# Kernel optimization log

Measured on AMD Instinct MI355X. Metric: run time of the kernel, lower is better.

Reference implementation:

```python
import jax, jax.numpy as jnp
import numpy as np

WBITS_MAX = 3.0   # 3-bit signed narrow-range weights: levels in [-3, 3]
ABITS_MAX = 15.0  # 4-bit unsigned activations: levels in [0, 15]


def round_ste(x):
    # straight-through estimator for round (Brevitas uses STE)
    return x + jax.lax.stop_gradient(jnp.round(x) - x)


def quant_weight(w):
    # per-tensor symmetric narrow-range 3-bit fake quant (Int weight per-tensor float)
    s = jnp.max(jnp.abs(w)) / WBITS_MAX
    wq = jnp.clip(round_ste(w / s), -WBITS_MAX, WBITS_MAX) * s
    return wq, s


def quant_bias(b, w_scale, in_step):
    # Brevitas BiasQuant: bias scale = input_scale * weight_scale, no clipping (wide int)
    sb = w_scale * in_step  # in_step is shape (1,)
    return round_ste(b / sb) * sb


def quant_relu(x, s):
    # QuantReLU(bit_width=4): relu then unsigned 4-bit fake quant with learned scale s
    step = s / ABITS_MAX
    return jnp.clip(round_ste(jax.nn.relu(x) / step), 0.0, ABITS_MAX) * step


def conv2d(x, w):
    return jax.lax.conv_general_dilated(
        x, w, window_strides=(1, 1), padding='VALID',
        dimension_numbers=('NCHW', 'OIHW', 'NCHW'))


def maxpool2(x):
    return jax.lax.reduce_window(x, -jnp.inf, jax.lax.max,
                                 (1, 1, 2, 2), (1, 1, 2, 2), 'VALID')


def setup_inputs() -> dict:
    key = jax.random.key(0)
    ks = jax.random.split(key, 16)
    d = {}
    d['x'] = jax.random.normal(ks[0], (256, 3, 160, 160), jnp.float32)
    d['w1'] = jax.random.normal(ks[1], (6, 3, 3, 3), jnp.float32) * 0.2
    d['w2'] = jax.random.normal(ks[2], (12, 6, 3, 3), jnp.float32) * 0.2
    d['b2'] = jax.random.normal(ks[3], (12,), jnp.float32) * 0.1
    d['w3'] = jax.random.normal(ks[4], (18, 12, 3, 3), jnp.float32) * 0.2
    d['b3'] = jax.random.normal(ks[5], (18,), jnp.float32) * 0.1
    d['w4'] = jax.random.normal(ks[6], (18, 18, 3, 3), jnp.float32) * 0.2
    d['b4'] = jax.random.normal(ks[7], (18,), jnp.float32) * 0.1
    d['w5'] = jax.random.normal(ks[8], (18, 18, 3, 3), jnp.float32) * 0.2
    d['b5'] = jax.random.normal(ks[9], (18,), jnp.float32) * 0.1
    d['fw1'] = jax.random.normal(ks[10], (120, 162), jnp.float32) * 0.1
    d['fb1'] = jax.random.normal(ks[11], (120,), jnp.float32) * 0.1
    d['fw2'] = jax.random.normal(ks[12], (84, 120), jnp.float32) * 0.1
    d['fb2'] = jax.random.normal(ks[13], (84,), jnp.float32) * 0.1
    d['fw3'] = jax.random.normal(ks[14], (9, 84), jnp.float32) * 0.1
    for i in range(1, 8):
        d[f's{i}'] = jnp.full((1,), 6.0, jnp.float32)  # learned act scales (calibrated init)
    return d


def reference(x, w1, w2, b2, w3, b3, w4, b4, w5, b5,
              fw1, fb1, fw2, fb2, fw3, s1, s2, s3, s4, s5, s6, s7):
    # stage 1 (note: original forward feeds raw x into conv1, bypassing quant_inp)
    q1, _ = quant_weight(w1)
    out = maxpool2(quant_relu(conv2d(x, q1), s1))            # [B,6,79,79]
    # stage 2
    q2, ws2 = quant_weight(w2)
    bq2 = quant_bias(b2, ws2, s1 / ABITS_MAX)
    out = maxpool2(quant_relu(conv2d(out, q2) + bq2[None, :, None, None], s2))  # [B,12,38,38]
    # stage 3
    q3, ws3 = quant_weight(w3)
    bq3 = quant_bias(b3, ws3, s2 / ABITS_MAX)
    out = maxpool2(quant_relu(conv2d(out, q3) + bq3[None, :, None, None], s3))  # [B,18,18,18]
    # stage 4
    q4, ws4 = quant_weight(w4)
    bq4 = quant_bias(b4, ws4, s3 / ABITS_MAX)
    out = maxpool2(quant_relu(conv2d(out, q4) + bq4[None, :, None, None], s4))  # [B,18,8,8]
    # stage 5
    q5, ws5 = quant_weight(w5)
    bq5 = quant_bias(b5, ws5, s4 / ABITS_MAX)
    out = maxpool2(quant_relu(conv2d(out, q5) + bq5[None, :, None, None], s5))  # [B,18,3,3]
    out = out.reshape(out.shape[0], -1)                      # [B,162]
    # fc1
    qf1, fs1 = quant_weight(fw1)
    bqf1 = quant_bias(fb1, fs1, s5 / ABITS_MAX)
    out = quant_relu(out @ qf1.T + bqf1, s6)                 # [B,120]
    # fc2
    qf2, fs2 = quant_weight(fw2)
    bqf2 = quant_bias(fb2, fs2, s6 / ABITS_MAX)
    out = quant_relu(out @ qf2.T + bqf2, s7)                 # [B,84]
    # fc3 (no bias, output not re-quantized: return_quant_tensor=False default path)
    qf3, _ = quant_weight(fw3)
    return out @ qf3.T                                       # [B,9]
```

## Files before the change

kernel.cpp:

```cpp
#include <hip/hip_runtime.h>
#include <hip/hip_bf16.h>
#include <math.h>
#include <type_traits>

constexpr size_t OFF_OUT1B = 0;
constexpr size_t OFF_OUT2B = (size_t)256 * 6 * 79 * 80;

template<int CIN, int COUT, int NCO, int HIN, int WSIN,
         int HPOOL, int WPOOL, int WSOUT, int XG, int RB,
         int THREADS, bool HAS_BIAS, bool IN_U8>
__global__ __launch_bounds__(THREADS)
void conv_stage(const void* __restrict__ in_,
                const float* __restrict__ w_raw,
                const float* __restrict__ b_raw,
                const float* __restrict__ s_prev,
                const float* __restrict__ s_act,
                unsigned char* __restrict__ out)
{
    using TIN = typename std::conditional<IN_U8, unsigned char, float>::type;
    constexpr int GROUPS = COUT / NCO;
    constexpr int W4IN   = WSIN / 4;
    constexpr int NW     = COUT * CIN * 9;
    constexpr int STEPS  = 4 * CIN;
    static_assert(NCO * GROUPS == COUT, "NCO divides COUT");
    static_assert(GROUPS * XG * RB <= THREADS, "single compute pass");
    static_assert(4 * XG == WSOUT, "full padded row coverage");
    static_assert(WSIN % 4 == 0, "vec4 loads");

    __shared__ float lw[NW];
    __shared__ float lb[COUT];
    __shared__ float red[THREADS];

    const int r0  = blockIdx.x * RB;
    const int n   = blockIdx.y;
    const int tid = threadIdx.x;

    float mx = 0.0f;
    for (int i = tid; i < NW; i += THREADS) {
        const float v = w_raw[i];
        lw[i] = v;
        mx = fmaxf(mx, fabsf(v));
    }
    if (HAS_BIAS)
        for (int i = tid; i < COUT; i += THREADS) lb[i] = b_raw[i];
    red[tid] = mx;
    __syncthreads();
    for (int s = THREADS / 2; s > 0; s >>= 1) {
        if (tid < s) red[tid] = fmaxf(red[tid], red[tid + s]);
        __syncthreads();
    }
    const float sw_ = red[0] / 3.0f;
    for (int i = tid; i < NW; i += THREADS) {
        float q = rintf(lw[i] / sw_);
        q = fminf(fmaxf(q, -3.0f), 3.0f);
        lw[i] = q * sw_;
    }
    if (HAS_BIAS) {
        const float sb = sw_ * (s_prev[0] / 15.0f);
        for (int i = tid; i < COUT; i += THREADS)
            lb[i] = rintf(lb[i] / sb) * sb;
    }
    __syncthreads();

    const int o = tid;
    if (o >= GROUPS * XG * RB) return;
    const int cog = o % GROUPS;
    const int xg  = (o / GROUPS) % XG;
    const int ry  = o / (GROUPS * XG);
    const int r   = r0 + ry;
    if (r >= HPOOL) return;

    const float step = s_act[0] / 15.0f;
    float step_in = 0.0f;
    if constexpr (IN_U8) step_in = s_prev[0] / 15.0f;

    const int u0 = 2 * xg;
    const int u1 = 2 * xg + 1;
    const int u2 = (2 * xg + 2 < W4IN) ? (2 * xg + 2) : (W4IN - 1);

    const TIN* in   = (const TIN*)in_;
    const TIN* base = in + (size_t)n * CIN * HIN * WSIN + (size_t)(2 * r) * WSIN;

    float acc[NCO][16];
#pragma unroll
    for (int j = 0; j < NCO; ++j)
#pragma unroll
        for (int i = 0; i < 16; ++i) acc[j][i] = 0.0f;

    float4       fbuf[3][3];
    unsigned int ubuf[3][3];
    float        wv[NCO][9];

#define ISSUE_STEP(S)                                                          \
    {                                                                          \
        const TIN* rp = base + (size_t)((S) >> 2) * HIN * WSIN                 \
                             + (size_t)((S) & 3) * WSIN;                       \
        if constexpr (IN_U8) {                                                 \
            ubuf[(S) % 3][0] = *(const unsigned int*)&rp[4 * u0];              \
            ubuf[(S) % 3][1] = *(const unsigned int*)&rp[4 * u1];              \
            ubuf[(S) % 3][2] = *(const unsigned int*)&rp[4 * u2];              \
        } else {                                                               \
            fbuf[(S) % 3][0] = *(const float4*)&rp[4 * u0];                    \
            fbuf[(S) % 3][1] = *(const float4*)&rp[4 * u1];                    \
            fbuf[(S) % 3][2] = *(const float4*)&rp[4 * u2];                    \
        }                                                                      \
    }

    ISSUE_STEP(0);
    ISSUE_STEP(1);

#pragma unroll
    for (int s = 0; s < STEPS; ++s) {
        const int c  = s >> 2;
        const int rr = s & 3;

        if (s + 2 < STEPS) ISSUE_STEP(s + 2);

        if (rr == 0) {
#pragma unroll
            for (int j = 0; j < NCO; ++j)
#pragma unroll
                for (int k = 0; k < 9; ++k)
                    wv[j][k] = lw[((NCO * cog + j) * CIN + c) * 9 + k];
        }

        float row[12];
        if constexpr (IN_U8) {
#pragma unroll
            for (int k = 0; k < 3; ++k) {
                const unsigned int d = ubuf[s % 3][k];
#pragma unroll
                for (int b = 0; b < 4; ++b)
                    row[4 * k + b] = (float)((d >> (8 * b)) & 0xffu) * step_in;
            }
        } else {
            const float* rv = (const float*)fbuf[s % 3];
#pragma unroll
            for (int i = 0; i < 12; ++i) row[i] = rv[i];
        }

        if (rr < 3) {
#pragma unroll
            for (int j = 0; j < NCO; ++j)
#pragma unroll
                for (int kc = 0; kc < 3; ++kc)
#pragma unroll
                    for (int xx = 0; xx < 8; ++xx)
                        acc[j][xx] = fmaf(row[xx + kc], wv[j][rr * 3 + kc], acc[j][xx]);
        }
        if (rr >= 1) {
#pragma unroll
            for (int j = 0; j < NCO; ++j)
#pragma unroll
                for (int kc = 0; kc < 3; ++kc)
#pragma unroll
                    for (int xx = 0; xx < 8; ++xx)
                        acc[j][8 + xx] = fmaf(row[xx + kc], wv[j][(rr - 1) * 3 + kc], acc[j][8 + xx]);
        }
    }
#undef ISSUE_STEP

#pragma unroll
    for (int j = 0; j < NCO; ++j) {
        const int co = NCO * cog + j;
        const float bias = HAS_BIAS ? lb[co] : 0.0f;
        unsigned int pck = 0;
#pragma unroll
        for (int t = 0; t < 4; ++t) {
            float m = fmaxf(fmaxf(acc[j][2 * t], acc[j][2 * t + 1]),
                            fmaxf(acc[j][8 + 2 * t], acc[j][8 + 2 * t + 1]));
            float v = fmaxf(m + bias, 0.0f);
            float q = rintf(v / step);
            q = fminf(fmaxf(q, 0.0f), 15.0f);
            const unsigned int qi = (4 * xg + t < WPOOL) ? (unsigned int)q : 0u;
            pck |= qi << (8 * t);
        }
        *(unsigned int*)&out[(((size_t)n * COUT + co) * HPOOL + r) * WSOUT + 4 * xg] = pck;
    }
}

__device__ __forceinline__ float wave_max(float v) {
#pragma unroll
    for (int off = 32; off > 0; off >>= 1)
        v = fmaxf(v, __shfl_down(v, off));
    return v;
}

__global__ __launch_bounds__(1024)
void tail_mega(const unsigned char* __restrict__ in2,
               const float* __restrict__ w3, const float* __restrict__ b3,
               const float* __restrict__ w4, const float* __restrict__ b4,
               const float* __restrict__ w5, const float* __restrict__ b5,
               const float* __restrict__ fw1, const float* __restrict__ fb1,
               const float* __restrict__ fw2, const float* __restrict__ fb2,
               const float* __restrict__ fw3,
               const float* __restrict__ s2, const float* __restrict__ s3,
               const float* __restrict__ s4, const float* __restrict__ s5,
               const float* __restrict__ s6, const float* __restrict__ s7,
               float* __restrict__ out)
{
    __shared__ unsigned int SLu[4560];
    __shared__ float A3[5832];
    __shared__ float W3q[1944], W4q[2916], W5q[2916];
    __shared__ float B3q[18], B4q[18], B5q[18];
    __shared__ float O4[1152];
    __shared__ float A5[162], A6[120], A7[84];
    __shared__ float sm[16][6];
    __shared__ float scales[6];

    const int n    = blockIdx.x;
    const int tid  = threadIdx.x;
    const int wid  = tid >> 6;
    const int lane = tid & 63;

    {
        const uint4* src = (const uint4*)(in2 + (size_t)n * 18240);
        uint4* dst = (uint4*)SLu;
        for (int i = tid; i < 1140; i += 1024) dst[i] = src[i];
    }
    float m3 = 0.f, m4 = 0.f, m5 = 0.f, g1 = 0.f, g2 = 0.f, g3 = 0.f;
    for (int i = tid; i < 1944; i += 1024) { const float v = w3[i]; W3q[i] = v; m3 = fmaxf(m3, fabsf(v)); }
    for (int i = tid; i < 2916; i += 1024) { const float v = w4[i]; W4q[i] = v; m4 = fmaxf(m4, fabsf(v)); }
    for (int i = tid; i < 2916; i += 1024) { const float v = w5[i]; W5q[i] = v; m5 = fmaxf(m5, fabsf(v)); }
    {
        const float4* f1 = (const float4*)fw1;
        for (int i = tid; i < 4860; i += 1024) {
            const float4 v = f1[i];
            g1 = fmaxf(g1, fmaxf(fmaxf(fabsf(v.x), fabsf(v.y)), fmaxf(fabsf(v.z), fabsf(v.w))));
        }
        const float4* f2 = (const float4*)fw2;
        for (int i = tid; i < 2520; i += 1024) {
            const float4 v = f2[i];
            g2 = fmaxf(g2, fmaxf(fmaxf(fabsf(v.x), fabsf(v.y)), fmaxf(fabsf(v.z), fabsf(v.w))));
        }
        const float4* f3 = (const float4*)fw3;
        for (int i = tid; i < 189; i += 1024) {
            const float4 v = f3[i];
            g3 = fmaxf(g3, fmaxf(fmaxf(fabsf(v.x), fabsf(v.y)), fmaxf(fabsf(v.z), fabsf(v.w))));
        }
    }
    if (tid < 18) { B3q[tid] = b3[tid]; B4q[tid] = b4[tid]; B5q[tid] = b5[tid]; }
    m3 = wave_max(m3); m4 = wave_max(m4); m5 = wave_max(m5);
    g1 = wave_max(g1); g2 = wave_max(g2); g3 = wave_max(g3);
    if (lane == 0) {
        sm[wid][0] = m3; sm[wid][1] = m4; sm[wid][2] = m5;
        sm[wid][3] = g1; sm[wid][4] = g2; sm[wid][5] = g3;
    }
    __syncthreads();
    if (tid < 6) {
        float v = sm[0][tid];
#pragma unroll
        for (int w = 1; w < 16; ++w) v = fmaxf(v, sm[w][tid]);
        scales[tid] = v / 3.0f;
    }
    __syncthreads();
    const float sw3 = scales[0], sw4 = scales[1], sw5 = scales[2];
    const float sf1 = scales[3], sf2 = scales[4], sf3 = scales[5];

    for (int i = tid; i < 1944; i += 1024) { float q = rintf(W3q[i] / sw3); q = fminf(fmaxf(q, -3.f), 3.f); W3q[i] = q * sw3; }
    for (int i = tid; i < 2916; i += 1024) { float q = rintf(W4q[i] / sw4); q = fminf(fmaxf(q, -3.f), 3.f); W4q[i] = q * sw4; }
    for (int i = tid; i < 2916; i += 1024) { float q = rintf(W5q[i] / sw5); q = fminf(fmaxf(q, -3.f), 3.f); W5q[i] = q * sw5; }
    if (tid < 18) {
        const float sb3 = sw3 * (s2[0] / 15.0f); B3q[tid] = rintf(B3q[tid] / sb3) * sb3;
        const float sb4 = sw4 * (s3[0] / 15.0f); B4q[tid] = rintf(B4q[tid] / sb4) * sb4;
        const float sb5 = sw5 * (s4[0] / 15.0f); B5q[tid] = rintf(B5q[tid] / sb5) * sb5;
    }
    __syncthreads();

    {
        const unsigned char* SLb = (const unsigned char*)SLu;
        const float step2 = s2[0] / 15.0f;
        const float st = s3[0] / 15.0f;
        if (tid < 972) {
            const int r  = tid / 54;
            const int rm = tid - r * 54;
            const int co = rm / 3;
            const int th = rm - co * 3;

            float acc0[12], acc1[12];
#pragma unroll
            for (int i = 0; i < 12; ++i) { acc0[i] = 0.f; acc1[i] = 0.f; }

            for (int c = 0; c < 12; ++c) {
                float wvv[9];
#pragma unroll
                for (int k = 0; k < 9; ++k) wvv[k] = W3q[(co * 12 + c) * 9 + k];
#pragma unroll
                for (int rr = 0; rr < 4; ++rr) {
                    const int off = (c * 38 + 2 * r + rr) * 40 + 12 * th;
                    float row[16];
#pragma unroll
                    for (int k = 0; k < 4; ++k) {
                        const unsigned int d = *(const unsigned int*)&SLb[off + 4 * k];
#pragma unroll
                        for (int b = 0; b < 4; ++b)
                            row[4 * k + b] = (float)((d >> (8 * b)) & 0xffu) * step2;
                    }
                    if (rr < 3) {
#pragma unroll
                        for (int kc = 0; kc < 3; ++kc)
#pragma unroll
                            for (int xx = 0; xx < 12; ++xx)
                                acc0[xx] = fmaf(row[xx + kc], wvv[rr * 3 + kc], acc0[xx]);
                    }
                    if (rr >= 1) {
#pragma unroll
                        for (int kc = 0; kc < 3; ++kc)
#pragma unroll
                            for (int xx = 0; xx < 12; ++xx)
                                acc1[xx] = fmaf(row[xx + kc], wvv[(rr - 1) * 3 + kc], acc1[xx]);
                    }
                }
            }
            const float bias = B3q[co];
#pragma unroll
            for (int x = 0; x < 6; ++x) {
                float m = fmaxf(fmaxf(acc0[2 * x], acc0[2 * x + 1]),
                                fmaxf(acc1[2 * x], acc1[2 * x + 1]));
                float v = fmaxf(m + bias, 0.0f);
                float q = rintf(v / st);
                q = fminf(fmaxf(q, 0.0f), 15.0f);
                A3[(co * 18 + r) * 18 + 6 * th + x] = q * st;
            }
        }
    }
    __syncthreads();

    {
        const float st = s4[0] / 15.0f;
        for (int o = tid; o < 1152; o += 1024) {
            const int co = o >> 6;
            const int r  = (o >> 3) & 7;
            const int x  = o & 7;
            float a00 = 0.f, a01 = 0.f, a10 = 0.f, a11 = 0.f;
            for (int c = 0; c < 18; ++c) {
                float win[4][4];
#pragma unroll
                for (int rr = 0; rr < 4; ++rr) {
                    const int base = c * 324 + (2 * r + rr) * 18 + 2 * x;
                    *(float2*)&win[rr][0] = *(const float2*)&A3[base];
                    *(float2*)&win[rr][2] = *(const float2*)&A3[base + 2];
                }
                const float* wp = &W4q[(co * 18 + c) * 9];
#pragma unroll
                for (int kr = 0; kr < 3; ++kr)
#pragma unroll
                    for (int kc = 0; kc < 3; ++kc) {
                        const float wvv = wp[kr * 3 + kc];
                        a00 = fmaf(win[kr    ][kc    ], wvv, a00);
                        a01 = fmaf(win[kr    ][kc + 1], wvv, a01);
                        a10 = fmaf(win[kr + 1][kc    ], wvv, a10);
                        a11 = fmaf(win[kr + 1][kc + 1], wvv, a11);
                    }
            }
            float m = fmaxf(fmaxf(a00, a01), fmaxf(a10, a11));
            float v = fmaxf(m + B4q[co], 0.0f);
            float q = rintf(v / st);
            q = fminf(fmaxf(q, 0.0f), 15.0f);
            O4[o] = q * st;
        }
    }
    __syncthreads();

    {
        const float st = s5[0] / 15.0f;
        if (tid < 162) {
            const int co  = tid / 9;
            const int rem = tid - co * 9;
            const int r   = rem / 3;
            const int x   = rem - r * 3;
            float a00 = 0.f, a01 = 0.f, a10 = 0.f, a11 = 0.f;
            for (int c = 0; c < 18; ++c) {
                float win[4][4];
#pragma unroll
                for (int rr = 0; rr < 4; ++rr) {
                    const int base = c * 64 + (2 * r + rr) * 8 + 2 * x;
                    *(float2*)&win[rr][0] = *(const float2*)&O4[base];
                    *(float2*)&win[rr][2] = *(const float2*)&O4[base + 2];
                }
                const float* wp = &W5q[(co * 18 + c) * 9];
#pragma unroll
                for (int kr = 0; kr < 3; ++kr)
#pragma unroll
                    for (int kc = 0; kc < 3; ++kc) {
                        const float wvv = wp[kr * 3 + kc];
                        a00 = fmaf(win[kr    ][kc    ], wvv, a00);
                        a01 = fmaf(win[kr    ][kc + 1], wvv, a01);
                        a10 = fmaf(win[kr + 1][kc    ], wvv, a10);
                        a11 = fmaf(win[kr + 1][kc + 1], wvv, a11);
                    }
            }
            float m = fmaxf(fmaxf(a00, a01), fmaxf(a10, a11));
            float v = fmaxf(m + B5q[co], 0.0f);
            float q = rintf(v / st);
            q = fminf(fmaxf(q, 0.0f), 15.0f);
            A5[tid] = q * st;
        }
    }
    __syncthreads();

    if (tid < 120) {
        float acc = 0.f;
        const float* wr = fw1 + (size_t)tid * 162;
#pragma unroll 6
        for (int k = 0; k < 162; ++k) {
            float q = rintf(wr[k] / sf1);
            q = fminf(fmaxf(q, -3.f), 3.f);
            acc = fmaf(A5[k], q * sf1, acc);
        }
        const float sb = sf1 * (s5[0] / 15.0f);
        acc += rintf(fb1[tid] / sb) * sb;
        const float st = s6[0] / 15.0f;
        float q = rintf(fmaxf(acc, 0.0f) / st);
        q = fminf(fmaxf(q, 0.0f), 15.0f);
        A6[tid] = q * st;
    }
    __syncthreads();

    if (tid < 84) {
        float acc = 0.f;
        const float* wr = fw2 + (size_t)tid * 120;
#pragma unroll 6
        for (int k = 0; k < 120; ++k) {
            float q = rintf(wr[k] / sf2);
            q = fminf(fmaxf(q, -3.f), 3.f);
            acc = fmaf(A6[k], q * sf2, acc);
        }
        const float sb = sf2 * (s6[0] / 15.0f);
        acc += rintf(fb2[tid] / sb) * sb;
        const float st = s7[0] / 15.0f;
        float q = rintf(fmaxf(acc, 0.0f) / st);
        q = fminf(fmaxf(q, 0.0f), 15.0f);
        A7[tid] = q * st;
    }
    __syncthreads();

    if (tid < 9) {
        float acc = 0.f;
        const float* wr = fw3 + (size_t)tid * 84;
#pragma unroll 6
        for (int k = 0; k < 84; ++k) {
            float q = rintf(wr[k] / sf3);
            q = fminf(fmaxf(q, -3.f), 3.f);
            acc = fmaf(A7[k], q * sf3, acc);
        }
        out[(size_t)n * 9 + tid] = acc;
    }
}

extern "C" void kernel_launch(void* const* d_in, const int* in_sizes, int n_in,
                              void* d_out, int out_size, void* d_ws, size_t ws_size,
                              hipStream_t stream)
{
    const float* x   = (const float*)d_in[0];
    const float* w1  = (const float*)d_in[1];
    const float* w2  = (const float*)d_in[2];
    const float* b2  = (const float*)d_in[3];
    const float* w3  = (const float*)d_in[4];
    const float* b3  = (const float*)d_in[5];
    const float* w4  = (const float*)d_in[6];
    const float* b4  = (const float*)d_in[7];
    const float* w5  = (const float*)d_in[8];
    const float* b5  = (const float*)d_in[9];
    const float* fw1 = (const float*)d_in[10];
    const float* fb1 = (const float*)d_in[11];
    const float* fw2 = (const float*)d_in[12];
    const float* fb2 = (const float*)d_in[13];
    const float* fw3 = (const float*)d_in[14];
    const float* s1  = (const float*)d_in[15];
    const float* s2  = (const float*)d_in[16];
    const float* s3  = (const float*)d_in[17];
    const float* s4  = (const float*)d_in[18];
    const float* s5  = (const float*)d_in[19];
    const float* s6  = (const float*)d_in[20];
    const float* s7  = (const float*)d_in[21];

    unsigned char* wsb = (unsigned char*)d_ws;
    float* out = (float*)d_out;

    conv_stage<3, 6, 2, 160, 160, 79, 79, 80, 20, 4, 256, false, false>
        <<<dim3(20, 256), 256, 0, stream>>>(x, w1, nullptr, nullptr, s1,
                                            wsb + OFF_OUT1B);

    conv_stage<6, 12, 2, 79, 80, 38, 38, 40, 10, 4, 256, true, true>
        <<<dim3(10, 256), 256, 0, stream>>>(wsb + OFF_OUT1B, w2, b2, s1, s2,
                                            wsb + OFF_OUT2B);

    tail_mega<<<256, 1024, 0, stream>>>(wsb + OFF_OUT2B,
                                        w3, b3, w4, b4, w5, b5,
                                        fw1, fb1, fw2, fb2, fw3,
                                        s2, s3, s4, s5, s6, s7, out);
}
```

Measured before the change: 138.9 us.

## Split stage-3 conv into its own kernel and parallelize FC layers across K-chunks

Moves the stage-3 convolution out of the per-image tail kernel into a separate kernel with two row blocks per image, so 512 blocks instead of 256 share the work. Inputs are decoded to float once in LDS and read as float4, and the results go to workspace as float. The remaining tail kernel reads A3 from global memory, stores O4 channel-last with padding, and splits the three FC dot products across up to 8 K-chunks with a shared-memory partial reduction. The cost is an extra launch and a float A3 round trip through global memory, and w3's absmax is recomputed in every block.

```diff
diff --git a/kernel.cpp b/kernel.cpp
--- a/kernel.cpp
+++ b/kernel.cpp
@@ -5,6 +5,7 @@
 
 constexpr size_t OFF_OUT1B = 0;
 constexpr size_t OFF_OUT2B = (size_t)256 * 6 * 79 * 80;
+constexpr size_t OFF_A3B   = 0;
 
 template<int CIN, int COUT, int NCO, int HIN, int WSIN,
          int HPOOL, int WPOOL, int WSOUT, int XG, int RB,
@@ -186,27 +187,138 @@
     return v;
 }
 
+__global__ __launch_bounds__(512)
+void conv3_stage(const unsigned char* __restrict__ in2,
+                 const float* __restrict__ w3, const float* __restrict__ b3,
+                 const float* __restrict__ s2, const float* __restrict__ s3,
+                 float* __restrict__ a3)
+{
+    __shared__ float SLf[12 * 20 * 40];
+    __shared__ float lw[1944];
+    __shared__ float lb[18];
+    __shared__ float red[512];
+
+    const int rb  = blockIdx.x;
+    const int n   = blockIdx.y;
+    const int tid = threadIdx.x;
+
+    float mx = 0.0f;
+    for (int i = tid; i < 1944; i += 512) {
+        const float v = w3[i];
+        lw[i] = v;
+        mx = fmaxf(mx, fabsf(v));
+    }
+    if (tid < 18) lb[tid] = b3[tid];
+    red[tid] = mx;
+
+    const float step2 = s2[0] / 15.0f;
+    {
+        const unsigned char* src = in2 + (size_t)n * 18240;
+        for (int d = tid; d < 2400; d += 512) {
+            const int c    = d / 200;
+            const int rem  = d - c * 200;
+            const int lrow = rem / 10;
+            const int dw   = rem - lrow * 10;
+            const unsigned int u =
+                *(const unsigned int*)&src[c * 1520 + (18 * rb + lrow) * 40 + 4 * dw];
+            float* q = &SLf[(c * 20 + lrow) * 40 + 4 * dw];
+            q[0] = (float)(u & 0xffu) * step2;
+            q[1] = (float)((u >> 8) & 0xffu) * step2;
+            q[2] = (float)((u >> 16) & 0xffu) * step2;
+            q[3] = (float)(u >> 24) * step2;
+        }
+    }
+    __syncthreads();
+    for (int s = 256; s > 0; s >>= 1) {
+        if (tid < s) red[tid] = fmaxf(red[tid], red[tid + s]);
+        __syncthreads();
+    }
+    const float sw = red[0] / 3.0f;
+    for (int i = tid; i < 1944; i += 512) {
+        float q = rintf(lw[i] / sw);
+        q = fminf(fmaxf(q, -3.0f), 3.0f);
+        lw[i] = q * sw;
+    }
+    if (tid < 18) {
+        const float sb = sw * (s2[0] / 15.0f);
+        lb[tid] = rintf(lb[tid] / sb) * sb;
+    }
+    __syncthreads();
+
+    if (tid >= 486) return;
+    const int rloc = tid / 54;
+    const int rm   = tid - rloc * 54;
+    const int co   = rm / 3;
+    const int th   = rm - co * 3;
+    const int r    = rb * 9 + rloc;
+
+    const float st = s3[0] / 15.0f;
+
+    float acc0[12], acc1[12];
+#pragma unroll
+    for (int i = 0; i < 12; ++i) { acc0[i] = 0.f; acc1[i] = 0.f; }
+
+    for (int c = 0; c < 12; ++c) {
+        float wv[9];
+#pragma unroll
+        for (int k = 0; k < 9; ++k) wv[k] = lw[(co * 12 + c) * 9 + k];
+#pragma unroll
+        for (int rr = 0; rr < 4; ++rr) {
+            const float* rp = &SLf[(c * 20 + 2 * rloc + rr) * 40 + 12 * th];
+            float4 rv[4];
+#pragma unroll
+            for (int v = 0; v < 4; ++v) rv[v] = *(const float4*)&rp[4 * v];
+            const float* row = (const float*)rv;
+            if (rr < 3) {
+#pragma unroll
+                for (int kc = 0; kc < 3; ++kc)
+#pragma unroll
+                    for (int xx = 0; xx < 12; ++xx)
+                        acc0[xx] = fmaf(row[xx + kc], wv[rr * 3 + kc], acc0[xx]);
+            }
+            if (rr >= 1) {
+#pragma unroll
+                for (int kc = 0; kc < 3; ++kc)
+#pragma unroll
+                    for (int xx = 0; xx < 12; ++xx)
+                        acc1[xx] = fmaf(row[xx + kc], wv[(rr - 1) * 3 + kc], acc1[xx]);
+            }
+        }
+    }
+
+    const float bias = lb[co];
+    float* orow = a3 + (size_t)n * 5832 + (size_t)co * 324 + (size_t)r * 18 + 6 * th;
+#pragma unroll
+    for (int x = 0; x < 6; ++x) {
+        float m = fmaxf(fmaxf(acc0[2 * x], acc0[2 * x + 1]),
+                        fmaxf(acc1[2 * x], acc1[2 * x + 1]));
+        float v = fmaxf(m + bias, 0.0f);
+        float q = rintf(v / st);
+        q = fminf(fmaxf(q, 0.0f), 15.0f);
+        orow[x] = q * st;
+    }
+}
+
 __global__ __launch_bounds__(1024)
-void tail_mega(const unsigned char* __restrict__ in2,
-               const float* __restrict__ w3, const float* __restrict__ b3,
-               const float* __restrict__ w4, const float* __restrict__ b4,
-               const float* __restrict__ w5, const float* __restrict__ b5,
-               const float* __restrict__ fw1, const float* __restrict__ fb1,
-               const float* __restrict__ fw2, const float* __restrict__ fb2,
-               const float* __restrict__ fw3,
-               const float* __restrict__ s2, const float* __restrict__ s3,
-               const float* __restrict__ s4, const float* __restrict__ s5,
-               const float* __restrict__ s6, const float* __restrict__ s7,
-               float* __restrict__ out)
+void tail456(const float* __restrict__ a3in,
+             const float* __restrict__ w4, const float* __restrict__ b4,
+             const float* __restrict__ w5, const float* __restrict__ b5,
+             const float* __restrict__ fw1, const float* __restrict__ fb1,
+             const float* __restrict__ fw2, const float* __restrict__ fb2,
+             const float* __restrict__ fw3,
+             const float* __restrict__ s3, const float* __restrict__ s4,
+             const float* __restrict__ s5, const float* __restrict__ s6,
+             const float* __restrict__ s7,
+             float* __restrict__ out)
 {
-    __shared__ unsigned int SLu[4560];
     __shared__ float A3[5832];
-    __shared__ float W3q[1944], W4q[2916], W5q[2916];
-    __shared__ float B3q[18], B4q[18], B5q[18];
-    __shared__ float O4[1152];
+    __shared__ float W4q[2916], W5q[2916];
+    __shared__ float B4q[18], B5q[18];
+    __shared__ float O4t[64 * 19 + 1];
     __shared__ float A5[162], A6[120], A7[84];
-    __shared__ float sm[16][6];
-    __shared__ float scales[6];
+    __shared__ float part[8][120];
+    __shared__ float sm[16][5];
+    __shared__ float scales[5];
 
     const int n    = blockIdx.x;
     const int tid  = threadIdx.x;
@@ -214,12 +326,11 @@
     const int lane = tid & 63;
 
     {
-        const uint4* src = (const uint4*)(in2 + (size_t)n * 18240);
-        uint4* dst = (uint4*)SLu;
-        for (int i = tid; i < 1140; i += 1024) dst[i] = src[i];
-    }
-    float m3 = 0.f, m4 = 0.f, m5 = 0.f, g1 = 0.f, g2 = 0.f, g3 = 0.f;
-    for (int i = tid; i < 1944; i += 1024) { const float v = w3[i]; W3q[i] = v; m3 = fmaxf(m3, fabsf(v)); }
+        const float4* src = (const float4*)(a3in + (size_t)n * 5832);
+        float4* dst = (float4*)A3;
+        for (int i = tid; i < 1458; i += 1024) dst[i] = src[i];
+    }
+    float m4 = 0.f, m5 = 0.f, g1 = 0.f, g2 = 0.f, g3 = 0.f;
     for (int i = tid; i < 2916; i += 1024) { const float v = w4[i]; W4q[i] = v; m4 = fmaxf(m4, fabsf(v)); }
     for (int i = tid; i < 2916; i += 1024) { const float v = w5[i]; W5q[i] = v; m5 = fmaxf(m5, fabsf(v)); }
     {
@@ -239,90 +350,29 @@
             g3 = fmaxf(g3, fmaxf(fmaxf(fabsf(v.x), fabsf(v.y)), fmaxf(fabsf(v.z), fabsf(v.w))));
         }
     }
-    if (tid < 18) { B3q[tid] = b3[tid]; B4q[tid] = b4[tid]; B5q[tid] = b5[tid]; }
-    m3 = wave_max(m3); m4 = wave_max(m4); m5 = wave_max(m5);
+    if (tid < 18) { B4q[tid] = b4[tid]; B5q[tid] = b5[tid]; }
+    m4 = wave_max(m4); m5 = wave_max(m5);
     g1 = wave_max(g1); g2 = wave_max(g2); g3 = wave_max(g3);
     if (lane == 0) {
-        sm[wid][0] = m3; sm[wid][1] = m4; sm[wid][2] = m5;
-        sm[wid][3] = g1; sm[wid][4] = g2; sm[wid][5] = g3;
-    }
-    __syncthreads();
-    if (tid < 6) {
+        sm[wid][0] = m4; sm[wid][1] = m5;
+        sm[wid][2] = g1; sm[wid][3] = g2; sm[wid][4] = g3;
+    }
+    __syncthreads();
+    if (tid < 5) {
         float v = sm[0][tid];
 #pragma unroll
         for (int w = 1; w < 16; ++w) v = fmaxf(v, sm[w][tid]);
         scales[tid] = v / 3.0f;
     }
     __syncthreads();
-    const float sw3 = scales[0], sw4 = scales[1], sw5 = scales[2];
-    const float sf1 = scales[3], sf2 = scales[4], sf3 = scales[5];
-
-    for (int i = tid; i < 1944; i += 1024) { float q = rintf(W3q[i] / sw3); q = fminf(fmaxf(q, -3.f), 3.f); W3q[i] = q * sw3; }
+    const float sw4 = scales[0], sw5 = scales[1];
+    const float sf1 = scales[2], sf2 = scales[3], sf3 = scales[4];
+
     for (int i = tid; i < 2916; i += 1024) { float q = rintf(W4q[i] / sw4); q = fminf(fmaxf(q, -3.f), 3.f); W4q[i] = q * sw4; }
     for (int i = tid; i < 2916; i += 1024) { float q = rintf(W5q[i] / sw5); q = fminf(fmaxf(q, -3.f), 3.f); W5q[i] = q * sw5; }
     if (tid < 18) {
-        const float sb3 = sw3 * (s2[0] / 15.0f); B3q[tid] = rintf(B3q[tid] / sb3) * sb3;
         const float sb4 = sw4 * (s3[0] / 15.0f); B4q[tid] = rintf(B4q[tid] / sb4) * sb4;
         const float sb5 = sw5 * (s4[0] / 15.0f); B5q[tid] = rintf(B5q[tid] / sb5) * sb5;
-    }
-    __syncthreads();
-
-    {
-        const unsigned char* SLb = (const unsigned char*)SLu;
-        const float step2 = s2[0] / 15.0f;
-        const float st = s3[0] / 15.0f;
-        if (tid < 972) {
-            const int r  = tid / 54;
-            const int rm = tid - r * 54;
-            const int co = rm / 3;
-            const int th = rm - co * 3;
-
-            float acc0[12], acc1[12];
-#pragma unroll
-            for (int i = 0; i < 12; ++i) { acc0[i] = 0.f; acc1[i] = 0.f; }
-
-            for (int c = 0; c < 12; ++c) {
-                float wvv[9];
-#pragma unroll
-                for (int k = 0; k < 9; ++k) wvv[k] = W3q[(co * 12 + c) * 9 + k];
-#pragma unroll
-                for (int rr = 0; rr < 4; ++rr) {
-                    const int off = (c * 38 + 2 * r + rr) * 40 + 12 * th;
-                    float row[16];
-#pragma unroll
-                    for (int k = 0; k < 4; ++k) {
-                        const unsigned int d = *(const unsigned int*)&SLb[off + 4 * k];
-#pragma unroll
-                        for (int b = 0; b < 4; ++b)
-                            row[4 * k + b] = (float)((d >> (8 * b)) & 0xffu) * step2;
-                    }
-                    if (rr < 3) {
-#pragma unroll
-                        for (int kc = 0; kc < 3; ++kc)
-#pragma unroll
-                            for (int xx = 0; xx < 12; ++xx)
-                                acc0[xx] = fmaf(row[xx + kc], wvv[rr * 3 + kc], acc0[xx]);
-                    }
-                    if (rr >= 1) {
-#pragma unroll
-                        for (int kc = 0; kc < 3; ++kc)
-#pragma unroll
-                            for (int xx = 0; xx < 12; ++xx)
-                                acc1[xx] = fmaf(row[xx + kc], wvv[(rr - 1) * 3 + kc], acc1[xx]);
-                    }
-                }
-            }
-            const float bias = B3q[co];
-#pragma unroll
-            for (int x = 0; x < 6; ++x) {
-                float m = fmaxf(fmaxf(acc0[2 * x], acc0[2 * x + 1]),
-                                fmaxf(acc1[2 * x], acc1[2 * x + 1]));
-                float v = fmaxf(m + bias, 0.0f);
-                float q = rintf(v / st);
-                q = fminf(fmaxf(q, 0.0f), 15.0f);
-                A3[(co * 18 + r) * 18 + 6 * th + x] = q * st;
-            }
-        }
     }
     __syncthreads();
 
@@ -357,7 +407,7 @@
             float v = fmaxf(m + B4q[co], 0.0f);
             float q = rintf(v / st);
             q = fminf(fmaxf(q, 0.0f), 15.0f);
-            O4[o] = q * st;
+            O4t[(r * 8 + x) * 19 + co] = q * st;
         }
     }
     __syncthreads();
@@ -373,11 +423,10 @@
             for (int c = 0; c < 18; ++c) {
                 float win[4][4];
 #pragma unroll
-                for (int rr = 0; rr < 4; ++rr) {
-                    const int base = c * 64 + (2 * r + rr) * 8 + 2 * x;
-                    *(float2*)&win[rr][0] = *(const float2*)&O4[base];
-                    *(float2*)&win[rr][2] = *(const float2*)&O4[base + 2];
-                }
+                for (int rr = 0; rr < 4; ++rr)
+#pragma unroll
+                    for (int cc = 0; cc < 4; ++cc)
+                        win[rr][cc] = O4t[((2 * r + rr) * 8 + 2 * x + cc) * 19 + c];
                 const float* wp = &W5q[(co * 18 + c) * 9];
 #pragma unroll
                 for (int kr = 0; kr < 3; ++kr)
@@ -399,15 +448,25 @@
     }
     __syncthreads();
 
-    if (tid < 120) {
-        float acc = 0.f;
-        const float* wr = fw1 + (size_t)tid * 162;
-#pragma unroll 6
-        for (int k = 0; k < 162; ++k) {
+    if (tid < 960) {
+        const int m  = tid % 120;
+        const int ch = tid / 120;
+        const int k0 = 21 * ch;
+        const int k1 = (ch == 7) ? 162 : k0 + 21;
+        float p = 0.f;
+        const float* wr = fw1 + (size_t)m * 162;
+        for (int k = k0; k < k1; ++k) {
             float q = rintf(wr[k] / sf1);
             q = fminf(fmaxf(q, -3.f), 3.f);
-            acc = fmaf(A5[k], q * sf1, acc);
-        }
+            p = fmaf(A5[k], q * sf1, p);
+        }
+        part[ch][m] = p;
+    }
+    __syncthreads();
+    if (tid < 120) {
+        float acc = part[0][tid];
+#pragma unroll
+        for (int ch = 1; ch < 8; ++ch) acc += part[ch][tid];
         const float sb = sf1 * (s5[0] / 15.0f);
         acc += rintf(fb1[tid] / sb) * sb;
         const float st = s6[0] / 15.0f;
@@ -417,15 +476,24 @@
     }
     __syncthreads();
 
-    if (tid < 84) {
-        float acc = 0.f;
-        const float* wr = fw2 + (size_t)tid * 120;
-#pragma unroll 6
-        for (int k = 0; k < 120; ++k) {
+    if (tid < 672) {
+        const int m  = tid % 84;
+        const int ch = tid / 84;
+        const int k0 = 15 * ch;
+        float p = 0.f;
+        const float* wr = fw2 + (size_t)m * 120;
+        for (int k = k0; k < k0 + 15; ++k) {
             float q = rintf(wr[k] / sf2);
             q = fminf(fmaxf(q, -3.f), 3.f);
-            acc = fmaf(A6[k], q * sf2, acc);
-        }
+            p = fmaf(A6[k], q * sf2, p);
+        }
+        part[ch][m] = p;
+    }
+    __syncthreads();
+    if (tid < 84) {
+        float acc = part[0][tid];
+#pragma unroll
+        for (int ch = 1; ch < 8; ++ch) acc += part[ch][tid];
         const float sb = sf2 * (s6[0] / 15.0f);
         acc += rintf(fb2[tid] / sb) * sb;
         const float st = s7[0] / 15.0f;
@@ -435,15 +503,24 @@
     }
     __syncthreads();
 
-    if (tid < 9) {
-        float acc = 0.f;
-        const float* wr = fw3 + (size_t)tid * 84;
-#pragma unroll 6
-        for (int k = 0; k < 84; ++k) {
+    if (tid < 63) {
+        const int m  = tid % 9;
+        const int ch = tid / 9;
+        const int k0 = 12 * ch;
+        float p = 0.f;
+        const float* wr = fw3 + (size_t)m * 84;
+        for (int k = k0; k < k0 + 12; ++k) {
             float q = rintf(wr[k] / sf3);
             q = fminf(fmaxf(q, -3.f), 3.f);
-            acc = fmaf(A7[k], q * sf3, acc);
-        }
+            p = fmaf(A7[k], q * sf3, p);
+        }
+        part[ch][m] = p;
+    }
+    __syncthreads();
+    if (tid < 9) {
+        float acc = part[0][tid];
+#pragma unroll
+        for (int ch = 1; ch < 7; ++ch) acc += part[ch][tid];
         out[(size_t)n * 9 + tid] = acc;
     }
 }
@@ -486,8 +563,11 @@
         <<<dim3(10, 256), 256, 0, stream>>>(wsb + OFF_OUT1B, w2, b2, s1, s2,
                                             wsb + OFF_OUT2B);
 
-    tail_mega<<<256, 1024, 0, stream>>>(wsb + OFF_OUT2B,
-                                        w3, b3, w4, b4, w5, b5,
-                                        fw1, fb1, fw2, fb2, fw3,
-                                        s2, s3, s4, s5, s6, s7, out);
+    conv3_stage<<<dim3(2, 256), 512, 0, stream>>>(wsb + OFF_OUT2B, w3, b3, s2, s3,
+                                                  (float*)(wsb + OFF_A3B));
+
+    tail456<<<256, 1024, 0, stream>>>((const float*)(wsb + OFF_A3B),
+                                      w4, b4, w5, b5,
+                                      fw1, fb1, fw2, fb2, fw3,
+                                      s3, s4, s5, s6, s7, out);
 }
```

Measured after the change: 141.8 us. +2.1%, slower.

## Stream stage-3 input from global with double buffering; split FC reductions across threads

Applied to the files above, without the earlier changes.

The tail kernel no longer stages the stage-2 activations in shared memory. Each thread loads its input rows straight from global memory into registers, double-buffered per input channel, so the loads overlap with the FMAs. The A3 and O4 shared arrays get padded or transposed layouts, and the three FC layers split their K dimension across up to 8 thread chunks with a shared-memory reduction. This cuts shared-memory footprint and the serial FC tail, at the cost of more registers and some uncoalesced global loads.

```diff
diff --git a/kernel.cpp b/kernel.cpp
--- a/kernel.cpp
+++ b/kernel.cpp
@@ -187,24 +187,24 @@
 }
 
 __global__ __launch_bounds__(1024)
-void tail_mega(const unsigned char* __restrict__ in2,
-               const float* __restrict__ w3, const float* __restrict__ b3,
-               const float* __restrict__ w4, const float* __restrict__ b4,
-               const float* __restrict__ w5, const float* __restrict__ b5,
-               const float* __restrict__ fw1, const float* __restrict__ fb1,
-               const float* __restrict__ fw2, const float* __restrict__ fb2,
-               const float* __restrict__ fw3,
-               const float* __restrict__ s2, const float* __restrict__ s3,
-               const float* __restrict__ s4, const float* __restrict__ s5,
-               const float* __restrict__ s6, const float* __restrict__ s7,
-               float* __restrict__ out)
+void tail_all(const unsigned char* __restrict__ in2,
+              const float* __restrict__ w3, const float* __restrict__ b3,
+              const float* __restrict__ w4, const float* __restrict__ b4,
+              const float* __restrict__ w5, const float* __restrict__ b5,
+              const float* __restrict__ fw1, const float* __restrict__ fb1,
+              const float* __restrict__ fw2, const float* __restrict__ fb2,
+              const float* __restrict__ fw3,
+              const float* __restrict__ s2, const float* __restrict__ s3,
+              const float* __restrict__ s4, const float* __restrict__ s5,
+              const float* __restrict__ s6, const float* __restrict__ s7,
+              float* __restrict__ out)
 {
-    __shared__ unsigned int SLu[4560];
-    __shared__ float A3[5832];
+    __shared__ float A3f[18 * 18 * 20];
     __shared__ float W3q[1944], W4q[2916], W5q[2916];
     __shared__ float B3q[18], B4q[18], B5q[18];
-    __shared__ float O4[1152];
+    __shared__ float O4t[64 * 19 + 1];
     __shared__ float A5[162], A6[120], A7[84];
+    __shared__ float part[8][120];
     __shared__ float sm[16][6];
     __shared__ float scales[6];
 
@@ -213,11 +213,6 @@
     const int wid  = tid >> 6;
     const int lane = tid & 63;
 
-    {
-        const uint4* src = (const uint4*)(in2 + (size_t)n * 18240);
-        uint4* dst = (uint4*)SLu;
-        for (int i = tid; i < 1140; i += 1024) dst[i] = src[i];
-    }
     float m3 = 0.f, m4 = 0.f, m5 = 0.f, g1 = 0.f, g2 = 0.f, g3 = 0.f;
     for (int i = tid; i < 1944; i += 1024) { const float v = w3[i]; W3q[i] = v; m3 = fmaxf(m3, fabsf(v)); }
     for (int i = tid; i < 2916; i += 1024) { const float v = w4[i]; W4q[i] = v; m4 = fmaxf(m4, fabsf(v)); }
@@ -267,61 +262,78 @@
     }
     __syncthreads();
 
-    {
-        const unsigned char* SLb = (const unsigned char*)SLu;
+    if (tid < 972) {
+        const int r  = tid / 54;
+        const int rm = tid - r * 54;
+        const int co = rm / 3;
+        const int th = rm - co * 3;
+
         const float step2 = s2[0] / 15.0f;
-        const float st = s3[0] / 15.0f;
-        if (tid < 972) {
-            const int r  = tid / 54;
-            const int rm = tid - r * 54;
-            const int co = rm / 3;
-            const int th = rm - co * 3;
-
-            float acc0[12], acc1[12];
-#pragma unroll
-            for (int i = 0; i < 12; ++i) { acc0[i] = 0.f; acc1[i] = 0.f; }
-
-            for (int c = 0; c < 12; ++c) {
-                float wvv[9];
-#pragma unroll
-                for (int k = 0; k < 9; ++k) wvv[k] = W3q[(co * 12 + c) * 9 + k];
-#pragma unroll
-                for (int rr = 0; rr < 4; ++rr) {
-                    const int off = (c * 38 + 2 * r + rr) * 40 + 12 * th;
-                    float row[16];
-#pragma unroll
-                    for (int k = 0; k < 4; ++k) {
-                        const unsigned int d = *(const unsigned int*)&SLb[off + 4 * k];
-#pragma unroll
-                        for (int b = 0; b < 4; ++b)
-                            row[4 * k + b] = (float)((d >> (8 * b)) & 0xffu) * step2;
-                    }
-                    if (rr < 3) {
-#pragma unroll
-                        for (int kc = 0; kc < 3; ++kc)
-#pragma unroll
-                            for (int xx = 0; xx < 12; ++xx)
-                                acc0[xx] = fmaf(row[xx + kc], wvv[rr * 3 + kc], acc0[xx]);
-                    }
-                    if (rr >= 1) {
-#pragma unroll
-                        for (int kc = 0; kc < 3; ++kc)
-#pragma unroll
-                            for (int xx = 0; xx < 12; ++xx)
-                                acc1[xx] = fmaf(row[xx + kc], wvv[(rr - 1) * 3 + kc], acc1[xx]);
-                    }
+        const float st3   = s3[0] / 15.0f;
+        const unsigned char* base = in2 + (size_t)n * 18240 + (size_t)(2 * r) * 40 + 12 * th;
+
+        float acc0[12], acc1[12];
+#pragma unroll
+        for (int i = 0; i < 12; ++i) { acc0[i] = 0.f; acc1[i] = 0.f; }
+
+        uint4 ub[2][4];
+
+#define LOADC(C, B)                                                            \
+        {                                                                      \
+            const unsigned char* cp = base + (size_t)(C) * 1520;               \
+            _Pragma("unroll")                                                  \
+            for (int rr = 0; rr < 4; ++rr)                                     \
+                __builtin_memcpy(&ub[B][rr], cp + rr * 40, 16);                \
+        }
+
+        LOADC(0, 0);
+
+#pragma unroll
+        for (int c = 0; c < 12; ++c) {
+            if (c + 1 < 12) LOADC(c + 1, (c + 1) & 1);
+
+            float wv[9];
+#pragma unroll
+            for (int k = 0; k < 9; ++k) wv[k] = W3q[(co * 12 + c) * 9 + k];
+
+#pragma unroll
+            for (int rr = 0; rr < 4; ++rr) {
+                const unsigned int* dp = (const unsigned int*)&ub[c & 1][rr];
+                float row[16];
+#pragma unroll
+                for (int k = 0; k < 4; ++k) {
+                    const unsigned int d = dp[k];
+#pragma unroll
+                    for (int b = 0; b < 4; ++b)
+                        row[4 * k + b] = (float)((d >> (8 * b)) & 0xffu) * step2;
+                }
+                if (rr < 3) {
+#pragma unroll
+                    for (int kc = 0; kc < 3; ++kc)
+#pragma unroll
+                        for (int xx = 0; xx < 12; ++xx)
+                            acc0[xx] = fmaf(row[xx + kc], wv[rr * 3 + kc], acc0[xx]);
+                }
+                if (rr >= 1) {
+#pragma unroll
+                    for (int kc = 0; kc < 3; ++kc)
+#pragma unroll
+                        for (int xx = 0; xx < 12; ++xx)
+                            acc1[xx] = fmaf(row[xx + kc], wv[(rr - 1) * 3 + kc], acc1[xx]);
                 }
             }
-            const float bias = B3q[co];
-#pragma unroll
-            for (int x = 0; x < 6; ++x) {
-                float m = fmaxf(fmaxf(acc0[2 * x], acc0[2 * x + 1]),
-                                fmaxf(acc1[2 * x], acc1[2 * x + 1]));
-                float v = fmaxf(m + bias, 0.0f);
-                float q = rintf(v / st);
-                q = fminf(fmaxf(q, 0.0f), 15.0f);
-                A3[(co * 18 + r) * 18 + 6 * th + x] = q * st;
-            }
+        }
+#undef LOADC
+
+        const float bias = B3q[co];
+#pragma unroll
+        for (int x = 0; x < 6; ++x) {
+            float m = fmaxf(fmaxf(acc0[2 * x], acc0[2 * x + 1]),
+                            fmaxf(acc1[2 * x], acc1[2 * x + 1]));
+            float v = fmaxf(m + bias, 0.0f);
+            float q = rintf(v / st3);
+            q = fminf(fmaxf(q, 0.0f), 15.0f);
+            A3f[(co * 18 + r) * 20 + 6 * th + x] = q * st3;
         }
     }
     __syncthreads();
@@ -337,9 +349,9 @@
                 float win[4][4];
 #pragma unroll
                 for (int rr = 0; rr < 4; ++rr) {
-                    const int base = c * 324 + (2 * r + rr) * 18 + 2 * x;
-                    *(float2*)&win[rr][0] = *(const float2*)&A3[base];
-                    *(float2*)&win[rr][2] = *(const float2*)&A3[base + 2];
+                    const int base = (c * 18 + 2 * r + rr) * 20 + 2 * x;
+                    *(float2*)&win[rr][0] = *(const float2*)&A3f[base];
+                    *(float2*)&win[rr][2] = *(const float2*)&A3f[base + 2];
                 }
                 const float* wp = &W4q[(co * 18 + c) * 9];
 #pragma unroll
@@ -357,7 +369,7 @@
             float v = fmaxf(m + B4q[co], 0.0f);
             float q = rintf(v / st);
             q = fminf(fmaxf(q, 0.0f), 15.0f);
-            O4[o] = q * st;
+            O4t[(r * 8 + x) * 19 + co] = q * st;
         }
     }
     __syncthreads();
@@ -373,11 +385,10 @@
             for (int c = 0; c < 18; ++c) {
                 float win[4][4];
 #pragma unroll
-                for (int rr = 0; rr < 4; ++rr) {
-                    const int base = c * 64 + (2 * r + rr) * 8 + 2 * x;
-                    *(float2*)&win[rr][0] = *(const float2*)&O4[base];
-                    *(float2*)&win[rr][2] = *(const float2*)&O4[base + 2];
-                }
+                for (int rr = 0; rr < 4; ++rr)
+#pragma unroll
+                    for (int cc = 0; cc < 4; ++cc)
+                        win[rr][cc] = O4t[((2 * r + rr) * 8 + 2 * x + cc) * 19 + c];
                 const float* wp = &W5q[(co * 18 + c) * 9];
 #pragma unroll
                 for (int kr = 0; kr < 3; ++kr)
@@ -399,15 +410,25 @@
     }
     __syncthreads();
 
-    if (tid < 120) {
-        float acc = 0.f;
-        const float* wr = fw1 + (size_t)tid * 162;
-#pragma unroll 6
-        for (int k = 0; k < 162; ++k) {
+    if (tid < 960) {
+        const int m  = tid % 120;
+        const int ch = tid / 120;
+        const int k0 = 21 * ch;
+        const int k1 = (ch == 7) ? 162 : k0 + 21;
+        float p = 0.f;
+        const float* wr = fw1 + (size_t)m * 162;
+        for (int k = k0; k < k1; ++k) {
             float q = rintf(wr[k] / sf1);
             q = fminf(fmaxf(q, -3.f), 3.f);
-            acc = fmaf(A5[k], q * sf1, acc);
-        }
+            p = fmaf(A5[k], q * sf1, p);
+        }
+        part[ch][m] = p;
+    }
+    __syncthreads();
+    if (tid < 120) {
+        float acc = part[0][tid];
+#pragma unroll
+        for (int ch = 1; ch < 8; ++ch) acc += part[ch][tid];
         const float sb = sf1 * (s5[0] / 15.0f);
         acc += rintf(fb1[tid] / sb) * sb;
         const float st = s6[0] / 15.0f;
@@ -417,15 +438,24 @@
     }
     __syncthreads();
 
-    if (tid < 84) {
-        float acc = 0.f;
-        const float* wr = fw2 + (size_t)tid * 120;
-#pragma unroll 6
-        for (int k = 0; k < 120; ++k) {
+    if (tid < 672) {
+        const int m  = tid % 84;
+        const int ch = tid / 84;
+        const int k0 = 15 * ch;
+        float p = 0.f;
+        const float* wr = fw2 + (size_t)m * 120;
+        for (int k = k0; k < k0 + 15; ++k) {
             float q = rintf(wr[k] / sf2);
             q = fminf(fmaxf(q, -3.f), 3.f);
-            acc = fmaf(A6[k], q * sf2, acc);
-        }
+            p = fmaf(A6[k], q * sf2, p);
+        }
+        part[ch][m] = p;
+    }
+    __syncthreads();
+    if (tid < 84) {
+        float acc = part[0][tid];
+#pragma unroll
+        for (int ch = 1; ch < 8; ++ch) acc += part[ch][tid];
         const float sb = sf2 * (s6[0] / 15.0f);
         acc += rintf(fb2[tid] / sb) * sb;
         const float st = s7[0] / 15.0f;
@@ -435,15 +465,24 @@
     }
     __syncthreads();
 
-    if (tid < 9) {
-        float acc = 0.f;
-        const float* wr = fw3 + (size_t)tid * 84;
-#pragma unroll 6
-        for (int k = 0; k < 84; ++k) {
+    if (tid < 63) {
+        const int m  = tid % 9;
+        const int ch = tid / 9;
+        const int k0 = 12 * ch;
+        float p = 0.f;
+        const float* wr = fw3 + (size_t)m * 84;
+        for (int k = k0; k < k0 + 12; ++k) {
             float q = rintf(wr[k] / sf3);
             q = fminf(fmaxf(q, -3.f), 3.f);
-            acc = fmaf(A7[k], q * sf3, acc);
-        }
+            p = fmaf(A7[k], q * sf3, p);
+        }
+        part[ch][m] = p;
+    }
+    __syncthreads();
+    if (tid < 9) {
+        float acc = part[0][tid];
+#pragma unroll
+        for (int ch = 1; ch < 7; ++ch) acc += part[ch][tid];
         out[(size_t)n * 9 + tid] = acc;
     }
 }
@@ -486,8 +525,8 @@
         <<<dim3(10, 256), 256, 0, stream>>>(wsb + OFF_OUT1B, w2, b2, s1, s2,
                                             wsb + OFF_OUT2B);
 
-    tail_mega<<<256, 1024, 0, stream>>>(wsb + OFF_OUT2B,
-                                        w3, b3, w4, b4, w5, b5,
-                                        fw1, fb1, fw2, fb2, fw3,
-                                        s2, s3, s4, s5, s6, s7, out);
+    tail_all<<<256, 1024, 0, stream>>>(wsb + OFF_OUT2B,
+                                       w3, b3, w4, b4, w5, b5,
+                                       fw1, fb1, fw2, fb2, fw3,
+                                       s2, s3, s4, s5, s6, s7, out);
 }
```

New measurement: 133.7 us. 1.04x faster.
